# Performance work log

Hardware: AMD Instinct MI355X
Metric: run time of the kernel (lower is better)

Reference implementation:

```python
import jax, jax.numpy as jnp
import numpy as np

N_NODES, E, M_CELLS = 100000, 400000, 50000
D_IN, D_H, D_OUT = 384, 256, 256


def setup_inputs() -> dict:
    key = jax.random.key(0)
    ks = jax.random.split(key, 13)
    s = 0.02
    return {
        "chunk_features": jax.random.normal(ks[0], (N_NODES, D_IN), jnp.float32),
        "flat_nodes_t": jax.random.randint(ks[1], (E,), 0, N_NODES),
        "cell_asgn_t": jax.random.randint(ks[2], (E,), 0, M_CELLS),
        "M": M_CELLS,
        # phi: Linear(D_IN,D_H)+ReLU, Linear(D_H,D_H)+ReLU
        "W1": jax.random.normal(ks[3], (D_IN, D_H), jnp.float32) * s,
        "b1": jnp.zeros((D_H,), jnp.float32),
        "W2": jax.random.normal(ks[4], (D_H, D_H), jnp.float32) * s,
        "b2": jnp.zeros((D_H,), jnp.float32),
        # rho: Linear(D_H,D_H)+ReLU, Linear(D_H,D_H)+ReLU, Linear(D_H,D_OUT)
        "R1": jax.random.normal(ks[5], (D_H, D_H), jnp.float32) * s,
        "c1": jnp.zeros((D_H,), jnp.float32),
        "R2": jax.random.normal(ks[6], (D_H, D_H), jnp.float32) * s,
        "c2": jnp.zeros((D_H,), jnp.float32),
        "R3": jax.random.normal(ks[7], (D_H, D_OUT), jnp.float32) * s,
        "c3": jnp.zeros((D_OUT,), jnp.float32),
    }


def reference(chunk_features, flat_nodes_t, cell_asgn_t, M,
              W1, b1, W2, b2, R1, c1, R2, c2, R3, c3):
    # gather node features per cell-membership: [E, D_IN]
    x = chunk_features[flat_nodes_t]
    # phi MLP
    h = jax.nn.relu(x @ W1 + b1)
    h = jax.nn.relu(h @ W2 + b2)            # [E, D_H]
    # scatter-add per cell (torch scatter_add_ into zeros)
    cell_sums = jax.ops.segment_sum(h, cell_asgn_t, num_segments=M)  # [M, D_H]
    # rho MLP
    r = jax.nn.relu(cell_sums @ R1 + c1)
    r = jax.nn.relu(r @ R2 + c2)
    return r @ R3 + c3                      # [M, D_OUT]
```

## Files before the change

kernel.cpp:

```cpp
#include <hip/hip_runtime.h>

typedef unsigned short u16;
typedef __bf16 bf16x8 __attribute__((ext_vector_type(8)));
typedef float f32x4 __attribute__((ext_vector_type(4)));

__device__ __forceinline__ u16 f2bf(float f) {
  unsigned int u = __builtin_bit_cast(unsigned int, f);
  u += 0x7fffu + ((u >> 16) & 1u);
  return (u16)(u >> 16);
}
__device__ __forceinline__ float bf2f(u16 h) {
  unsigned int u = ((unsigned int)h) << 16;
  return __builtin_bit_cast(float, u);
}

__global__ __launch_bounds__(256) void k_prep(
    const float* __restrict__ W1, const float* __restrict__ W2,
    const float* __restrict__ R1, const float* __restrict__ R2, const float* __restrict__ R3,
    u16* __restrict__ W1s, u16* __restrict__ W2s,
    u16* __restrict__ R1s, u16* __restrict__ R2s, u16* __restrict__ R3s) {
  int t = blockIdx.x * 256 + threadIdx.x;
  const float* src; u16* dst; int lt;
  if (t < 12288) { src = W1; dst = W1s; lt = t; }
  else {
    int u = t - 12288;
    int m = u >> 13;
    lt = u & 8191;
    if (m == 0)      { src = W2; dst = W2s; }
    else if (m == 1) { src = R1; dst = R1s; }
    else if (m == 2) { src = R2; dst = R2s; }
    else if (m == 3) { src = R3; dst = R3s; }
    else return;
  }
  int lane = lt & 63;
  int nt = (lt >> 6) & 15;
  int ks = lt >> 10;
  int col = nt * 16 + (lane & 15);
  int kb = ks * 32 + (lane >> 4) * 8;
  union { u16 u[8]; uint4 v; } o;
#pragma unroll
  for (int j = 0; j < 8; ++j) o.u[j] = f2bf(src[(size_t)(kb + j) * 256 + col]);
  *(uint4*)(dst + (size_t)lt * 8) = o.v;
}

__global__ __launch_bounds__(256) void k_hist(const int* __restrict__ cells,
                                              int* __restrict__ counts, int E) {
  int e = blockIdx.x * 256 + threadIdx.x;
  if (e < E) atomicAdd(&counts[cells[e]], 1);
}

__global__ __launch_bounds__(256) void k_scan1(const int* __restrict__ counts,
                                               int* __restrict__ offs,
                                               int* __restrict__ bsum, int M) {
  __shared__ int ws[4];
  int tid = threadIdx.x, lane = tid & 63, wid = tid >> 6;
  int i = blockIdx.x * 256 + tid;
  int v = (i < M) ? counts[i] : 0;
  int x = v;
#pragma unroll
  for (int s = 1; s < 64; s <<= 1) { int y = __shfl_up(x, s); if (lane >= s) x += y; }
  if (lane == 63) ws[wid] = x;
  __syncthreads();
  int pre = 0;
#pragma unroll
  for (int w = 0; w < 4; ++w) if (w < wid) pre += ws[w];
  if (i < M) offs[i] = pre + x - v;
  if (tid == 255) bsum[blockIdx.x] = pre + x;
}

__global__ __launch_bounds__(256) void k_scan2(int* __restrict__ bsum, int nb) {
  __shared__ int ws[4];
  int tid = threadIdx.x, lane = tid & 63, wid = tid >> 6;
  int v = (tid < nb) ? bsum[tid] : 0;
  int x = v;
#pragma unroll
  for (int s = 1; s < 64; s <<= 1) { int y = __shfl_up(x, s); if (lane >= s) x += y; }
  if (lane == 63) ws[wid] = x;
  __syncthreads();
  int pre = 0;
#pragma unroll
  for (int w = 0; w < 4; ++w) if (w < wid) pre += ws[w];
  if (tid < nb) bsum[tid] = pre + x - v;
}

__global__ __launch_bounds__(256) void k_scan3(int* __restrict__ offs,
                                               const int* __restrict__ bsum,
                                               int* __restrict__ cursor, int M, int E) {
  int i = blockIdx.x * 256 + threadIdx.x;
  if (i < M) { int o = offs[i] + bsum[blockIdx.x]; offs[i] = o; cursor[i] = o; }
  if (i == M) offs[M] = E;
}

__global__ __launch_bounds__(256) void k_scatter(const int* __restrict__ cells,
                                                 const int* __restrict__ nodes,
                                                 int* __restrict__ cursor,
                                                 int* __restrict__ sorted, int E) {
  int e = blockIdx.x * 256 + threadIdx.x;
  if (e < E) {
    int c = cells[e];
    int p = atomicAdd(&cursor[c], 1);
    sorted[p] = nodes[e];
  }
}

__global__ __launch_bounds__(256) void k_phi(
    const float* __restrict__ X,
    const u16* __restrict__ W1s, const float* __restrict__ b1,
    const u16* __restrict__ W2s, const float* __restrict__ b2,
    u16* __restrict__ H, int N) {
  __shared__ __align__(16) u16 xbuf[32 * 384];
  __shared__ __align__(16) u16 hbuf[32 * 256];
  const int tid = threadIdx.x, lane = tid & 63, wid = tid >> 6;
  const int g = lane >> 4, r16 = lane & 15;
  const int swz = r16 << 3;
  const int T = (N + 31) >> 5;
  const int step = gridDim.x;

  const u16* w1p = W1s + (size_t)(wid * 4) * 512 + lane * 8;
  const u16* w2p = W2s + (size_t)(wid * 4) * 512 + lane * 8;

  float bias1[4], bias2[4];
#pragma unroll
  for (int n = 0; n < 4; ++n) {
    bias1[n] = b1[wid * 64 + n * 16 + r16];
    bias2[n] = b2[wid * 64 + n * 16 + r16];
  }

  f32x4 xr[12];

  auto issue = [&](int t) {
#pragma unroll
    for (int it = 0; it < 12; ++it) {
      int u = it * 256 + tid;
      int row = u / 96, c4 = u - row * 96;
      int crow = t * 32 + row; crow = crow < N ? crow : N - 1;
      xr[it] = *(const f32x4*)(X + (size_t)crow * 384 + c4 * 4);
    }
  };
  auto stagewrite = [&]() {
#pragma unroll
    for (int it = 0; it < 12; ++it) {
      int u = it * 256 + tid;
      int row = u / 96, c4 = u - row * 96;
      uint2 pk;
      pk.x = (unsigned int)f2bf(xr[it][0]) | ((unsigned int)f2bf(xr[it][1]) << 16);
      pk.y = (unsigned int)f2bf(xr[it][2]) | ((unsigned int)f2bf(xr[it][3]) << 16);
      *(uint2*)(xbuf + row * 384 + ((c4 * 4) ^ ((row & 15) << 3))) = pk;
    }
  };

  const int t0 = blockIdx.x;
  if (t0 >= T) return;

  issue(t0);
  stagewrite();
  __syncthreads();
  issue(t0 + step);

  for (int t = t0; t < T; t += step) {
    f32x4 acc[2][4];
#pragma unroll
    for (int m = 0; m < 2; ++m)
#pragma unroll
      for (int n = 0; n < 4; ++n) acc[m][n] = (f32x4){0.f, 0.f, 0.f, 0.f};
#pragma unroll 4
    for (int ks = 0; ks < 12; ++ks) {
      bf16x8 bfr[4];
#pragma unroll
      for (int n = 0; n < 4; ++n)
        bfr[n] = *(const bf16x8*)(w1p + (size_t)ks * 8192 + n * 512);
      const u16* bp = xbuf + ((ks * 32 + g * 8) ^ swz);
#pragma unroll
      for (int m = 0; m < 2; ++m) {
        bf16x8 af = *(const bf16x8*)(bp + (m * 16 + r16) * 384);
#pragma unroll
        for (int n = 0; n < 4; ++n)
          acc[m][n] = __builtin_amdgcn_mfma_f32_16x16x32_bf16(af, bfr[n], acc[m][n], 0, 0, 0);
      }
    }
    __syncthreads();

    stagewrite();

#pragma unroll
    for (int m = 0; m < 2; ++m)
#pragma unroll
      for (int n = 0; n < 4; ++n)
#pragma unroll
        for (int rr = 0; rr < 4; ++rr) {
          int row = m * 16 + g * 4 + rr;
          int col = wid * 64 + n * 16 + r16;
          float v = fmaxf(acc[m][n][rr] + bias1[n], 0.f);
          hbuf[row * 256 + (col ^ ((row & 15) << 3))] = f2bf(v);
        }
    __syncthreads();

    issue(t + 2 * step);

#pragma unroll
    for (int m = 0; m < 2; ++m)
#pragma unroll
      for (int n = 0; n < 4; ++n) acc[m][n] = (f32x4){0.f, 0.f, 0.f, 0.f};
#pragma unroll 4
    for (int ks = 0; ks < 8; ++ks) {
      bf16x8 bfr[4];
#pragma unroll
      for (int n = 0; n < 4; ++n)
        bfr[n] = *(const bf16x8*)(w2p + (size_t)ks * 8192 + n * 512);
      const u16* bp = hbuf + ((ks * 32 + g * 8) ^ swz);
#pragma unroll
      for (int m = 0; m < 2; ++m) {
        bf16x8 af = *(const bf16x8*)(bp + (m * 16 + r16) * 256);
#pragma unroll
        for (int n = 0; n < 4; ++n)
          acc[m][n] = __builtin_amdgcn_mfma_f32_16x16x32_bf16(af, bfr[n], acc[m][n], 0, 0, 0);
      }
    }
    __syncthreads();

#pragma unroll
    for (int m = 0; m < 2; ++m)
#pragma unroll
      for (int n = 0; n < 4; ++n)
#pragma unroll
        for (int rr = 0; rr < 4; ++rr) {
          int row = m * 16 + g * 4 + rr;
          int col = wid * 64 + n * 16 + r16;
          float v = fmaxf(acc[m][n][rr] + bias2[n], 0.f);
          hbuf[row * 256 + (col ^ ((row & 15) << 3))] = f2bf(v);
        }
    __syncthreads();

#pragma unroll
    for (int it = 0; it < 4; ++it) {
      int u = it * 256 + tid;
      int row = u >> 5, k8 = u & 31;
      uint4 d = *(const uint4*)(hbuf + row * 256 + ((k8 * 8) ^ ((row & 15) << 3)));
      int grow = t * 32 + row;
      if (grow < N) *(uint4*)(H + (size_t)grow * 256 + k8 * 8) = d;
    }
  }
}

__global__ __launch_bounds__(256) void k_cellsum(
    const u16* __restrict__ H, const int* __restrict__ sorted,
    const int* __restrict__ offs, u16* __restrict__ CS, int M) {
  const int lane = threadIdx.x & 63, wid = threadIdx.x >> 6;
  int c = blockIdx.x * 4 + wid;
  if (c >= M) return;
  int s = offs[c], e = offs[c + 1];
  float a0 = 0.f, a1 = 0.f, a2 = 0.f, a3 = 0.f;
  for (int base = s; base < e; base += 64) {
    int cnt = e - base; if (cnt > 64) cnt = 64;
    int idx = sorted[base + (lane < cnt ? lane : 0)];
    int j = 0;
    for (; j + 8 <= cnt; j += 8) {
      ushort4 h[8];
#pragma unroll
      for (int q = 0; q < 8; ++q) {
        int nd = __shfl(idx, j + q);
        h[q] = *(const ushort4*)(H + (size_t)nd * 256 + lane * 4);
      }
#pragma unroll
      for (int q = 0; q < 8; ++q) {
        a0 += bf2f(h[q].x); a1 += bf2f(h[q].y);
        a2 += bf2f(h[q].z); a3 += bf2f(h[q].w);
      }
    }
    if (j + 4 <= cnt) {
      ushort4 h[4];
#pragma unroll
      for (int q = 0; q < 4; ++q) {
        int nd = __shfl(idx, j + q);
        h[q] = *(const ushort4*)(H + (size_t)nd * 256 + lane * 4);
      }
#pragma unroll
      for (int q = 0; q < 4; ++q) {
        a0 += bf2f(h[q].x); a1 += bf2f(h[q].y);
        a2 += bf2f(h[q].z); a3 += bf2f(h[q].w);
      }
      j += 4;
    }
    for (; j < cnt; ++j) {
      int nd = __shfl(idx, j);
      ushort4 h = *(const ushort4*)(H + (size_t)nd * 256 + lane * 4);
      a0 += bf2f(h.x); a1 += bf2f(h.y); a2 += bf2f(h.z); a3 += bf2f(h.w);
    }
  }
  ushort4 o;
  o.x = f2bf(a0); o.y = f2bf(a1); o.z = f2bf(a2); o.w = f2bf(a3);
  *(ushort4*)(CS + (size_t)c * 256 + lane * 4) = o;
}

__global__ __launch_bounds__(256) void k_rho(
    const u16* __restrict__ CS,
    const u16* __restrict__ R1s, const float* __restrict__ c1,
    const u16* __restrict__ R2s, const float* __restrict__ c2,
    const u16* __restrict__ R3s, const float* __restrict__ c3,
    float* __restrict__ OUT, int M) {
  __shared__ __align__(16) u16 xbuf[32 * 256];
  __shared__ __align__(16) u16 hbuf[32 * 256];
  const int tid = threadIdx.x, lane = tid & 63, wid = tid >> 6;
  const int g = lane >> 4, r16 = lane & 15;
  const int swz = r16 << 3;
  const int T = (M + 31) >> 5;
  const int step = gridDim.x;

  const u16* w1p = R1s + (size_t)(wid * 4) * 512 + lane * 8;
  const u16* w2p = R2s + (size_t)(wid * 4) * 512 + lane * 8;
  const u16* w3p = R3s + (size_t)(wid * 4) * 512 + lane * 8;

  float bias1[4], bias2[4], bias3[4];
#pragma unroll
  for (int n = 0; n < 4; ++n) {
    bias1[n] = c1[wid * 64 + n * 16 + r16];
    bias2[n] = c2[wid * 64 + n * 16 + r16];
    bias3[n] = c3[wid * 64 + n * 16 + r16];
  }

  uint4 xr[4];
  auto issue = [&](int t) {
#pragma unroll
    for (int it = 0; it < 4; ++it) {
      int u = it * 256 + tid;
      int row = u >> 5, k8 = u & 31;
      int crow = t * 32 + row; crow = crow < M ? crow : M - 1;
      xr[it] = *(const uint4*)(CS + (size_t)crow * 256 + k8 * 8);
    }
  };
  auto stagewrite = [&]() {
#pragma unroll
    for (int it = 0; it < 4; ++it) {
      int u = it * 256 + tid;
      int row = u >> 5, k8 = u & 31;
      *(uint4*)(xbuf + row * 256 + ((k8 * 8) ^ ((row & 15) << 3))) = xr[it];
    }
  };

  const int t0 = blockIdx.x;
  if (t0 >= T) return;
  issue(t0);
  stagewrite();
  __syncthreads();
  issue(t0 + step);

  for (int t = t0; t < T; t += step) {
    f32x4 acc[2][4];

#pragma unroll
    for (int m = 0; m < 2; ++m)
#pragma unroll
      for (int n = 0; n < 4; ++n) acc[m][n] = (f32x4){0.f, 0.f, 0.f, 0.f};
#pragma unroll 4
    for (int ks = 0; ks < 8; ++ks) {
      bf16x8 bfr[4];
#pragma unroll
      for (int n = 0; n < 4; ++n)
        bfr[n] = *(const bf16x8*)(w1p + (size_t)ks * 8192 + n * 512);
      const u16* bp = xbuf + ((ks * 32 + g * 8) ^ swz);
#pragma unroll
      for (int m = 0; m < 2; ++m) {
        bf16x8 af = *(const bf16x8*)(bp + (m * 16 + r16) * 256);
#pragma unroll
        for (int n = 0; n < 4; ++n)
          acc[m][n] = __builtin_amdgcn_mfma_f32_16x16x32_bf16(af, bfr[n], acc[m][n], 0, 0, 0);
      }
    }
    __syncthreads();

    stagewrite();

#pragma unroll
    for (int m = 0; m < 2; ++m)
#pragma unroll
      for (int n = 0; n < 4; ++n)
#pragma unroll
        for (int rr = 0; rr < 4; ++rr) {
          int row = m * 16 + g * 4 + rr;
          int col = wid * 64 + n * 16 + r16;
          float v = fmaxf(acc[m][n][rr] + bias1[n], 0.f);
          hbuf[row * 256 + (col ^ ((row & 15) << 3))] = f2bf(v);
        }
    __syncthreads();

    issue(t + 2 * step);

#pragma unroll
    for (int m = 0; m < 2; ++m)
#pragma unroll
      for (int n = 0; n < 4; ++n) acc[m][n] = (f32x4){0.f, 0.f, 0.f, 0.f};
#pragma unroll 4
    for (int ks = 0; ks < 8; ++ks) {
      bf16x8 bfr[4];
#pragma unroll
      for (int n = 0; n < 4; ++n)
        bfr[n] = *(const bf16x8*)(w2p + (size_t)ks * 8192 + n * 512);
      const u16* bp = hbuf + ((ks * 32 + g * 8) ^ swz);
#pragma unroll
      for (int m = 0; m < 2; ++m) {
        bf16x8 af = *(const bf16x8*)(bp + (m * 16 + r16) * 256);
#pragma unroll
        for (int n = 0; n < 4; ++n)
          acc[m][n] = __builtin_amdgcn_mfma_f32_16x16x32_bf16(af, bfr[n], acc[m][n], 0, 0, 0);
      }
    }
    __syncthreads();

#pragma unroll
    for (int m = 0; m < 2; ++m)
#pragma unroll
      for (int n = 0; n < 4; ++n)
#pragma unroll
        for (int rr = 0; rr < 4; ++rr) {
          int row = m * 16 + g * 4 + rr;
          int col = wid * 64 + n * 16 + r16;
          float v = fmaxf(acc[m][n][rr] + bias2[n], 0.f);
          hbuf[row * 256 + (col ^ ((row & 15) << 3))] = f2bf(v);
        }
    __syncthreads();

#pragma unroll
    for (int m = 0; m < 2; ++m)
#pragma unroll
      for (int n = 0; n < 4; ++n) acc[m][n] = (f32x4){0.f, 0.f, 0.f, 0.f};
#pragma unroll 4
    for (int ks = 0; ks < 8; ++ks) {
      bf16x8 bfr[4];
#pragma unroll
      for (int n = 0; n < 4; ++n)
        bfr[n] = *(const bf16x8*)(w3p + (size_t)ks * 8192 + n * 512);
      const u16* bp = hbuf + ((ks * 32 + g * 8) ^ swz);
#pragma unroll
      for (int m = 0; m < 2; ++m) {
        bf16x8 af = *(const bf16x8*)(bp + (m * 16 + r16) * 256);
#pragma unroll
        for (int n = 0; n < 4; ++n)
          acc[m][n] = __builtin_amdgcn_mfma_f32_16x16x32_bf16(af, bfr[n], acc[m][n], 0, 0, 0);
      }
    }
#pragma unroll
    for (int n = 0; n < 4; ++n) {
#pragma unroll
      for (int m = 0; m < 2; ++m)
#pragma unroll
        for (int rr = 0; rr < 4; ++rr) {
          int grow = t * 32 + m * 16 + g * 4 + rr;
          if (grow < M)
            OUT[(size_t)grow * 256 + wid * 64 + n * 16 + r16] = acc[m][n][rr] + bias3[n];
        }
    }
  }
}

extern "C" void kernel_launch(void* const* d_in, const int* in_sizes, int n_in,
                              void* d_out, int out_size, void* d_ws, size_t ws_size,
                              hipStream_t stream) {
  const float* X    = (const float*)d_in[0];
  const int* nodes  = (const int*)d_in[1];
  const int* cells  = (const int*)d_in[2];
  const float* W1   = (const float*)d_in[4];
  const float* b1   = (const float*)d_in[5];
  const float* W2   = (const float*)d_in[6];
  const float* b2   = (const float*)d_in[7];
  const float* R1   = (const float*)d_in[8];
  const float* c1   = (const float*)d_in[9];
  const float* R2   = (const float*)d_in[10];
  const float* c2   = (const float*)d_in[11];
  const float* R3   = (const float*)d_in[12];
  const float* c3   = (const float*)d_in[13];
  float* OUT = (float*)d_out;

  const int N = in_sizes[0] / 384;
  const int E = in_sizes[1];
  const int M = out_size / 256;

  char* ws = (char*)d_ws;
  size_t off = 0;
  auto alloc = [&](size_t b) { size_t o = off; off += (b + 255) & ~(size_t)255; return o; };
  u16* W1s    = (u16*)(ws + alloc((size_t)12 * 16 * 64 * 8 * 2));
  u16* W2s    = (u16*)(ws + alloc((size_t)8 * 16 * 64 * 8 * 2));
  u16* R1s    = (u16*)(ws + alloc((size_t)8 * 16 * 64 * 8 * 2));
  u16* R2s    = (u16*)(ws + alloc((size_t)8 * 16 * 64 * 8 * 2));
  u16* R3s    = (u16*)(ws + alloc((size_t)8 * 16 * 64 * 8 * 2));
  u16* H      = (u16*)(ws + alloc((size_t)N * 256 * 2));
  u16* CS     = (u16*)(ws + alloc((size_t)M * 256 * 2));
  int* counts = (int*)(ws + alloc((size_t)M * 4));
  int* offs   = (int*)(ws + alloc((size_t)(M + 1) * 4));
  int* cursor = (int*)(ws + alloc((size_t)M * 4));
  int* sorted = (int*)(ws + alloc((size_t)E * 4));
  int* bsum   = (int*)(ws + alloc((size_t)256 * 4));

  const int NB = (M + 255) / 256;

  hipMemsetAsync(counts, 0, (size_t)M * 4, stream);
  k_prep<<<176, 256, 0, stream>>>(W1, W2, R1, R2, R3, W1s, W2s, R1s, R2s, R3s);
  k_hist<<<(E + 255) / 256, 256, 0, stream>>>(cells, counts, E);
  k_scan1<<<NB, 256, 0, stream>>>(counts, offs, bsum, M);
  k_scan2<<<1, 256, 0, stream>>>(bsum, NB);
  k_scan3<<<(M + 256) / 256, 256, 0, stream>>>(offs, bsum, cursor, M, E);
  k_scatter<<<(E + 255) / 256, 256, 0, stream>>>(cells, nodes, cursor, sorted, E);
  k_phi<<<1024, 256, 0, stream>>>(X, W1s, b1, W2s, b2, H, N);
  k_cellsum<<<(M + 3) / 4, 256, 0, stream>>>(H, sorted, offs, CS, M);
  k_rho<<<512, 256, 0, stream>>>(CS, R1s, c1, R2s, c2, R3s, c3, OUT, M);
}
```

Before: 219.0 us.

## Split phi MLP into two persistent kernels with weights resident in LDS

The fused phi kernel is split into two persistent kernels, one per layer, each running 256 blocks at one block per CU. Each block copies its layer's bf16 weights into shared memory (the last third of W1 is held in registers), so weights no longer have to be re-read from global or L2 on every tile. The price is an extra round trip of the N×256 bf16 intermediate through global memory, an extra launch, and lower occupancy that leaves less latency hiding.

```diff
diff --git a/kernel.cpp b/kernel.cpp
--- a/kernel.cpp
+++ b/kernel.cpp
@@ -103,31 +103,36 @@
   }
 }
 
-__global__ __launch_bounds__(256) void k_phi(
+__global__ __launch_bounds__(256, 1) void k_phi_l1(
     const float* __restrict__ X,
     const u16* __restrict__ W1s, const float* __restrict__ b1,
-    const u16* __restrict__ W2s, const float* __restrict__ b2,
-    u16* __restrict__ H, int N) {
+    u16* __restrict__ P, int N) {
+  __shared__ __align__(16) u16 wlds[65536];
   __shared__ __align__(16) u16 xbuf[32 * 384];
-  __shared__ __align__(16) u16 hbuf[32 * 256];
   const int tid = threadIdx.x, lane = tid & 63, wid = tid >> 6;
   const int g = lane >> 4, r16 = lane & 15;
   const int swz = r16 << 3;
   const int T = (N + 31) >> 5;
   const int step = gridDim.x;
 
-  const u16* w1p = W1s + (size_t)(wid * 4) * 512 + lane * 8;
-  const u16* w2p = W2s + (size_t)(wid * 4) * 512 + lane * 8;
-
-  float bias1[4], bias2[4];
-#pragma unroll
-  for (int n = 0; n < 4; ++n) {
-    bias1[n] = b1[wid * 64 + n * 16 + r16];
-    bias2[n] = b2[wid * 64 + n * 16 + r16];
-  }
+  {
+    const uint4* wsrc = (const uint4*)W1s;
+    uint4* wdst = (uint4*)wlds;
+#pragma unroll
+    for (int i = 0; i < 32; ++i) wdst[i * 256 + tid] = wsrc[i * 256 + tid];
+  }
+  bf16x8 ksr[4][4];
+#pragma unroll
+  for (int k2 = 0; k2 < 4; ++k2)
+#pragma unroll
+    for (int n = 0; n < 4; ++n)
+      ksr[k2][n] = *(const bf16x8*)(W1s + ((size_t)((8 + k2) * 16 + wid * 4 + n) * 64 + lane) * 8);
+
+  float bias1[4];
+#pragma unroll
+  for (int n = 0; n < 4; ++n) bias1[n] = b1[wid * 64 + n * 16 + r16];
 
   f32x4 xr[12];
-
   auto issue = [&](int t) {
 #pragma unroll
     for (int it = 0; it < 12; ++it) {
@@ -151,24 +156,25 @@
 
   const int t0 = blockIdx.x;
   if (t0 >= T) return;
-
   issue(t0);
-  stagewrite();
-  __syncthreads();
-  issue(t0 + step);
 
   for (int t = t0; t < T; t += step) {
+    stagewrite();
+    __syncthreads();
+    issue(t + step);
+
     f32x4 acc[2][4];
 #pragma unroll
     for (int m = 0; m < 2; ++m)
 #pragma unroll
       for (int n = 0; n < 4; ++n) acc[m][n] = (f32x4){0.f, 0.f, 0.f, 0.f};
-#pragma unroll 4
-    for (int ks = 0; ks < 12; ++ks) {
+
+#pragma unroll 2
+    for (int ks = 0; ks < 8; ++ks) {
       bf16x8 bfr[4];
 #pragma unroll
       for (int n = 0; n < 4; ++n)
-        bfr[n] = *(const bf16x8*)(w1p + (size_t)ks * 8192 + n * 512);
+        bfr[n] = *(const bf16x8*)(wlds + ((ks * 16 + wid * 4 + n) * 64 + lane) * 8);
       const u16* bp = xbuf + ((ks * 32 + g * 8) ^ swz);
 #pragma unroll
       for (int m = 0; m < 2; ++m) {
@@ -178,9 +184,18 @@
           acc[m][n] = __builtin_amdgcn_mfma_f32_16x16x32_bf16(af, bfr[n], acc[m][n], 0, 0, 0);
       }
     }
-    __syncthreads();
-
-    stagewrite();
+#pragma unroll
+    for (int k2 = 0; k2 < 4; ++k2) {
+      const u16* bp = xbuf + (((8 + k2) * 32 + g * 8) ^ swz);
+#pragma unroll
+      for (int m = 0; m < 2; ++m) {
+        bf16x8 af = *(const bf16x8*)(bp + (m * 16 + r16) * 384);
+#pragma unroll
+        for (int n = 0; n < 4; ++n)
+          acc[m][n] = __builtin_amdgcn_mfma_f32_16x16x32_bf16(af, ksr[k2][n], acc[m][n], 0, 0, 0);
+      }
+    }
+    __syncthreads();
 
 #pragma unroll
     for (int m = 0; m < 2; ++m)
@@ -191,23 +206,83 @@
           int row = m * 16 + g * 4 + rr;
           int col = wid * 64 + n * 16 + r16;
           float v = fmaxf(acc[m][n][rr] + bias1[n], 0.f);
-          hbuf[row * 256 + (col ^ ((row & 15) << 3))] = f2bf(v);
+          xbuf[row * 256 + (col ^ ((row & 15) << 3))] = f2bf(v);
         }
     __syncthreads();
 
-    issue(t + 2 * step);
-
+#pragma unroll
+    for (int it = 0; it < 4; ++it) {
+      int u = it * 256 + tid;
+      int row = u >> 5, k8 = u & 31;
+      uint4 d = *(const uint4*)(xbuf + row * 256 + ((k8 * 8) ^ ((row & 15) << 3)));
+      int grow = t * 32 + row;
+      if (grow < N) *(uint4*)(P + (size_t)grow * 256 + k8 * 8) = d;
+    }
+    __syncthreads();
+  }
+}
+
+__global__ __launch_bounds__(256, 1) void k_phi_l2(
+    const u16* __restrict__ W2s, const float* __restrict__ b2,
+    u16* __restrict__ P, int N) {
+  __shared__ __align__(16) u16 wlds[65536];
+  __shared__ __align__(16) u16 xbuf[32 * 256];
+  const int tid = threadIdx.x, lane = tid & 63, wid = tid >> 6;
+  const int g = lane >> 4, r16 = lane & 15;
+  const int swz = r16 << 3;
+  const int T = (N + 31) >> 5;
+  const int step = gridDim.x;
+
+  {
+    const uint4* wsrc = (const uint4*)W2s;
+    uint4* wdst = (uint4*)wlds;
+#pragma unroll
+    for (int i = 0; i < 32; ++i) wdst[i * 256 + tid] = wsrc[i * 256 + tid];
+  }
+  float bias2[4];
+#pragma unroll
+  for (int n = 0; n < 4; ++n) bias2[n] = b2[wid * 64 + n * 16 + r16];
+
+  uint4 xr[4];
+  auto issue = [&](int t) {
+#pragma unroll
+    for (int it = 0; it < 4; ++it) {
+      int u = it * 256 + tid;
+      int row = u >> 5, k8 = u & 31;
+      int crow = t * 32 + row; crow = crow < N ? crow : N - 1;
+      xr[it] = *(const uint4*)(P + (size_t)crow * 256 + k8 * 8);
+    }
+  };
+  auto stagewrite = [&]() {
+#pragma unroll
+    for (int it = 0; it < 4; ++it) {
+      int u = it * 256 + tid;
+      int row = u >> 5, k8 = u & 31;
+      *(uint4*)(xbuf + row * 256 + ((k8 * 8) ^ ((row & 15) << 3))) = xr[it];
+    }
+  };
+
+  const int t0 = blockIdx.x;
+  if (t0 >= T) return;
+  issue(t0);
+
+  for (int t = t0; t < T; t += step) {
+    stagewrite();
+    __syncthreads();
+    issue(t + step);
+
+    f32x4 acc[2][4];
 #pragma unroll
     for (int m = 0; m < 2; ++m)
 #pragma unroll
       for (int n = 0; n < 4; ++n) acc[m][n] = (f32x4){0.f, 0.f, 0.f, 0.f};
-#pragma unroll 4
+#pragma unroll 2
     for (int ks = 0; ks < 8; ++ks) {
       bf16x8 bfr[4];
 #pragma unroll
       for (int n = 0; n < 4; ++n)
-        bfr[n] = *(const bf16x8*)(w2p + (size_t)ks * 8192 + n * 512);
-      const u16* bp = hbuf + ((ks * 32 + g * 8) ^ swz);
+        bfr[n] = *(const bf16x8*)(wlds + ((ks * 16 + wid * 4 + n) * 64 + lane) * 8);
+      const u16* bp = xbuf + ((ks * 32 + g * 8) ^ swz);
 #pragma unroll
       for (int m = 0; m < 2; ++m) {
         bf16x8 af = *(const bf16x8*)(bp + (m * 16 + r16) * 256);
@@ -227,7 +302,7 @@
           int row = m * 16 + g * 4 + rr;
           int col = wid * 64 + n * 16 + r16;
           float v = fmaxf(acc[m][n][rr] + bias2[n], 0.f);
-          hbuf[row * 256 + (col ^ ((row & 15) << 3))] = f2bf(v);
+          xbuf[row * 256 + (col ^ ((row & 15) << 3))] = f2bf(v);
         }
     __syncthreads();
 
@@ -235,10 +310,11 @@
     for (int it = 0; it < 4; ++it) {
       int u = it * 256 + tid;
       int row = u >> 5, k8 = u & 31;
-      uint4 d = *(const uint4*)(hbuf + row * 256 + ((k8 * 8) ^ ((row & 15) << 3)));
+      uint4 d = *(const uint4*)(xbuf + row * 256 + ((k8 * 8) ^ ((row & 15) << 3)));
       int grow = t * 32 + row;
-      if (grow < N) *(uint4*)(H + (size_t)grow * 256 + k8 * 8) = d;
-    }
+      if (grow < N) *(uint4*)(P + (size_t)grow * 256 + k8 * 8) = d;
+    }
+    __syncthreads();
   }
 }
 
@@ -482,7 +558,7 @@
   u16* R1s    = (u16*)(ws + alloc((size_t)8 * 16 * 64 * 8 * 2));
   u16* R2s    = (u16*)(ws + alloc((size_t)8 * 16 * 64 * 8 * 2));
   u16* R3s    = (u16*)(ws + alloc((size_t)8 * 16 * 64 * 8 * 2));
-  u16* H      = (u16*)(ws + alloc((size_t)N * 256 * 2));
+  u16* P      = (u16*)(ws + alloc((size_t)N * 256 * 2));
   u16* CS     = (u16*)(ws + alloc((size_t)M * 256 * 2));
   int* counts = (int*)(ws + alloc((size_t)M * 4));
   int* offs   = (int*)(ws + alloc((size_t)(M + 1) * 4));
@@ -499,7 +575,8 @@
   k_scan2<<<1, 256, 0, stream>>>(bsum, NB);
   k_scan3<<<(M + 256) / 256, 256, 0, stream>>>(offs, bsum, cursor, M, E);
   k_scatter<<<(E + 255) / 256, 256, 0, stream>>>(cells, nodes, cursor, sorted, E);
-  k_phi<<<1024, 256, 0, stream>>>(X, W1s, b1, W2s, b2, H, N);
-  k_cellsum<<<(M + 3) / 4, 256, 0, stream>>>(H, sorted, offs, CS, M);
+  k_phi_l1<<<256, 256, 0, stream>>>(X, W1s, b1, P, N);
+  k_phi_l2<<<256, 256, 0, stream>>>(W2s, b2, P, N);
+  k_cellsum<<<(M + 3) / 4, 256, 0, stream>>>(P, sorted, offs, CS, M);
   k_rho<<<512, 256, 0, stream>>>(CS, R1s, c1, R2s, c2, R3s, c3, OUT, M);
 }
```

Result: slower. 247.9 us (+13.2%).

## Split fused phi and rho MLP kernels into per-layer non-persistent kernels

Applied to the files above, without the earlier changes.

Replaces the persistent, software-prefetched k_phi and k_rho kernels with one kernel per linear layer (k_l1, k_b2b, k_lout), each processing a single 32-row tile per block. Intermediate activations are now round-tripped through global bf16 buffers (h1buf, RB) instead of staying in shared memory. The aim is likely higher occupancy, since each kernel uses less LDS and a simpler body. The cost is extra global memory traffic, more launches, loss of load/compute overlap, and narrow scattered bf16 stores. One launch also passes RB as both source and destination of a __restrict__ kernel.

```diff
diff --git a/kernel.cpp b/kernel.cpp
--- a/kernel.cpp
+++ b/kernel.cpp
@@ -103,41 +103,27 @@
   }
 }
 
-__global__ __launch_bounds__(256) void k_phi(
+__global__ __launch_bounds__(256) void k_l1(
     const float* __restrict__ X,
     const u16* __restrict__ W1s, const float* __restrict__ b1,
-    const u16* __restrict__ W2s, const float* __restrict__ b2,
-    u16* __restrict__ H, int N) {
+    u16* __restrict__ h1, int N) {
   __shared__ __align__(16) u16 xbuf[32 * 384];
-  __shared__ __align__(16) u16 hbuf[32 * 256];
   const int tid = threadIdx.x, lane = tid & 63, wid = tid >> 6;
   const int g = lane >> 4, r16 = lane & 15;
   const int swz = r16 << 3;
-  const int T = (N + 31) >> 5;
-  const int step = gridDim.x;
-
-  const u16* w1p = W1s + (size_t)(wid * 4) * 512 + lane * 8;
-  const u16* w2p = W2s + (size_t)(wid * 4) * 512 + lane * 8;
-
-  float bias1[4], bias2[4];
-#pragma unroll
-  for (int n = 0; n < 4; ++n) {
-    bias1[n] = b1[wid * 64 + n * 16 + r16];
-    bias2[n] = b2[wid * 64 + n * 16 + r16];
-  }
-
-  f32x4 xr[12];
-
-  auto issue = [&](int t) {
+  const int rbase = blockIdx.x * 32;
+
+  const u16* wp = W1s + (size_t)(wid * 4) * 512 + lane * 8;
+
+  {
+    f32x4 xr[12];
 #pragma unroll
     for (int it = 0; it < 12; ++it) {
       int u = it * 256 + tid;
       int row = u / 96, c4 = u - row * 96;
-      int crow = t * 32 + row; crow = crow < N ? crow : N - 1;
+      int crow = rbase + row; crow = crow < N ? crow : N - 1;
       xr[it] = *(const f32x4*)(X + (size_t)crow * 384 + c4 * 4);
     }
-  };
-  auto stagewrite = [&]() {
 #pragma unroll
     for (int it = 0; it < 12; ++it) {
       int u = it * 256 + tid;
@@ -147,99 +133,184 @@
       pk.y = (unsigned int)f2bf(xr[it][2]) | ((unsigned int)f2bf(xr[it][3]) << 16);
       *(uint2*)(xbuf + row * 384 + ((c4 * 4) ^ ((row & 15) << 3))) = pk;
     }
-  };
-
-  const int t0 = blockIdx.x;
-  if (t0 >= T) return;
-
-  issue(t0);
-  stagewrite();
+  }
   __syncthreads();
-  issue(t0 + step);
-
-  for (int t = t0; t < T; t += step) {
-    f32x4 acc[2][4];
-#pragma unroll
-    for (int m = 0; m < 2; ++m)
-#pragma unroll
-      for (int n = 0; n < 4; ++n) acc[m][n] = (f32x4){0.f, 0.f, 0.f, 0.f};
+
+  f32x4 acc[2][4];
+#pragma unroll
+  for (int m = 0; m < 2; ++m)
+#pragma unroll
+    for (int n = 0; n < 4; ++n) acc[m][n] = (f32x4){0.f, 0.f, 0.f, 0.f};
+
 #pragma unroll 4
-    for (int ks = 0; ks < 12; ++ks) {
-      bf16x8 bfr[4];
+  for (int ks = 0; ks < 12; ++ks) {
+    bf16x8 bfr[4];
+#pragma unroll
+    for (int n = 0; n < 4; ++n)
+      bfr[n] = *(const bf16x8*)(wp + (size_t)ks * 8192 + n * 512);
+    const u16* bp = xbuf + ((ks * 32 + g * 8) ^ swz);
+#pragma unroll
+    for (int m = 0; m < 2; ++m) {
+      bf16x8 af = *(const bf16x8*)(bp + (m * 16 + r16) * 384);
 #pragma unroll
       for (int n = 0; n < 4; ++n)
-        bfr[n] = *(const bf16x8*)(w1p + (size_t)ks * 8192 + n * 512);
-      const u16* bp = xbuf + ((ks * 32 + g * 8) ^ swz);
-#pragma unroll
-      for (int m = 0; m < 2; ++m) {
-        bf16x8 af = *(const bf16x8*)(bp + (m * 16 + r16) * 384);
+        acc[m][n] = __builtin_amdgcn_mfma_f32_16x16x32_bf16(af, bfr[n], acc[m][n], 0, 0, 0);
+    }
+  }
+
+  float bias[4];
+#pragma unroll
+  for (int n = 0; n < 4; ++n) bias[n] = b1[wid * 64 + n * 16 + r16];
+#pragma unroll
+  for (int m = 0; m < 2; ++m)
+#pragma unroll
+    for (int rr = 0; rr < 4; ++rr) {
+      int grow = rbase + m * 16 + g * 4 + rr;
+      if (grow < N) {
+        u16* op = h1 + (size_t)grow * 256 + wid * 64 + r16;
 #pragma unroll
         for (int n = 0; n < 4; ++n)
-          acc[m][n] = __builtin_amdgcn_mfma_f32_16x16x32_bf16(af, bfr[n], acc[m][n], 0, 0, 0);
-      }
-    }
-    __syncthreads();
-
-    stagewrite();
-
-#pragma unroll
-    for (int m = 0; m < 2; ++m)
+          op[n * 16] = f2bf(fmaxf(acc[m][n][rr] + bias[n], 0.f));
+      }
+    }
+}
+
+__global__ __launch_bounds__(256) void k_b2b(
+    const u16* __restrict__ src,
+    const u16* __restrict__ Ws, const float* __restrict__ b,
+    u16* __restrict__ dst, int R) {
+  __shared__ __align__(16) u16 xbuf[32 * 256];
+  const int tid = threadIdx.x, lane = tid & 63, wid = tid >> 6;
+  const int g = lane >> 4, r16 = lane & 15;
+  const int swz = r16 << 3;
+  const int rbase = blockIdx.x * 32;
+
+  const u16* wp = Ws + (size_t)(wid * 4) * 512 + lane * 8;
+
+  {
+    uint4 xr[4];
+#pragma unroll
+    for (int it = 0; it < 4; ++it) {
+      int u = it * 256 + tid;
+      int row = u >> 5, k8 = u & 31;
+      int crow = rbase + row; crow = crow < R ? crow : R - 1;
+      xr[it] = *(const uint4*)(src + (size_t)crow * 256 + k8 * 8);
+    }
+#pragma unroll
+    for (int it = 0; it < 4; ++it) {
+      int u = it * 256 + tid;
+      int row = u >> 5, k8 = u & 31;
+      *(uint4*)(xbuf + row * 256 + ((k8 * 8) ^ ((row & 15) << 3))) = xr[it];
+    }
+  }
+  __syncthreads();
+
+  f32x4 acc[2][4];
+#pragma unroll
+  for (int m = 0; m < 2; ++m)
+#pragma unroll
+    for (int n = 0; n < 4; ++n) acc[m][n] = (f32x4){0.f, 0.f, 0.f, 0.f};
+
+#pragma unroll 4
+  for (int ks = 0; ks < 8; ++ks) {
+    bf16x8 bfr[4];
+#pragma unroll
+    for (int n = 0; n < 4; ++n)
+      bfr[n] = *(const bf16x8*)(wp + (size_t)ks * 8192 + n * 512);
+    const u16* bp = xbuf + ((ks * 32 + g * 8) ^ swz);
+#pragma unroll
+    for (int m = 0; m < 2; ++m) {
+      bf16x8 af = *(const bf16x8*)(bp + (m * 16 + r16) * 256);
 #pragma unroll
       for (int n = 0; n < 4; ++n)
-#pragma unroll
-        for (int rr = 0; rr < 4; ++rr) {
-          int row = m * 16 + g * 4 + rr;
-          int col = wid * 64 + n * 16 + r16;
-          float v = fmaxf(acc[m][n][rr] + bias1[n], 0.f);
-          hbuf[row * 256 + (col ^ ((row & 15) << 3))] = f2bf(v);
-        }
-    __syncthreads();
-
-    issue(t + 2 * step);
-
-#pragma unroll
-    for (int m = 0; m < 2; ++m)
-#pragma unroll
-      for (int n = 0; n < 4; ++n) acc[m][n] = (f32x4){0.f, 0.f, 0.f, 0.f};
+        acc[m][n] = __builtin_amdgcn_mfma_f32_16x16x32_bf16(af, bfr[n], acc[m][n], 0, 0, 0);
+    }
+  }
+
+  float bias[4];
+#pragma unroll
+  for (int n = 0; n < 4; ++n) bias[n] = b[wid * 64 + n * 16 + r16];
+#pragma unroll
+  for (int m = 0; m < 2; ++m)
+#pragma unroll
+    for (int rr = 0; rr < 4; ++rr) {
+      int grow = rbase + m * 16 + g * 4 + rr;
+      if (grow < R) {
+        u16* op = dst + (size_t)grow * 256 + wid * 64 + r16;
+#pragma unroll
+        for (int n = 0; n < 4; ++n)
+          op[n * 16] = f2bf(fmaxf(acc[m][n][rr] + bias[n], 0.f));
+      }
+    }
+}
+
+__global__ __launch_bounds__(256) void k_lout(
+    const u16* __restrict__ src,
+    const u16* __restrict__ Ws, const float* __restrict__ b,
+    float* __restrict__ OUT, int R) {
+  __shared__ __align__(16) u16 xbuf[32 * 256];
+  const int tid = threadIdx.x, lane = tid & 63, wid = tid >> 6;
+  const int g = lane >> 4, r16 = lane & 15;
+  const int swz = r16 << 3;
+  const int rbase = blockIdx.x * 32;
+
+  const u16* wp = Ws + (size_t)(wid * 4) * 512 + lane * 8;
+
+  {
+    uint4 xr[4];
+#pragma unroll
+    for (int it = 0; it < 4; ++it) {
+      int u = it * 256 + tid;
+      int row = u >> 5, k8 = u & 31;
+      int crow = rbase + row; crow = crow < R ? crow : R - 1;
+      xr[it] = *(const uint4*)(src + (size_t)crow * 256 + k8 * 8);
+    }
+#pragma unroll
+    for (int it = 0; it < 4; ++it) {
+      int u = it * 256 + tid;
+      int row = u >> 5, k8 = u & 31;
+      *(uint4*)(xbuf + row * 256 + ((k8 * 8) ^ ((row & 15) << 3))) = xr[it];
+    }
+  }
+  __syncthreads();
+
+  f32x4 acc[2][4];
+#pragma unroll
+  for (int m = 0; m < 2; ++m)
+#pragma unroll
+    for (int n = 0; n < 4; ++n) acc[m][n] = (f32x4){0.f, 0.f, 0.f, 0.f};
+
 #pragma unroll 4
-    for (int ks = 0; ks < 8; ++ks) {
-      bf16x8 bfr[4];
+  for (int ks = 0; ks < 8; ++ks) {
+    bf16x8 bfr[4];
+#pragma unroll
+    for (int n = 0; n < 4; ++n)
+      bfr[n] = *(const bf16x8*)(wp + (size_t)ks * 8192 + n * 512);
+    const u16* bp = xbuf + ((ks * 32 + g * 8) ^ swz);
+#pragma unroll
+    for (int m = 0; m < 2; ++m) {
+      bf16x8 af = *(const bf16x8*)(bp + (m * 16 + r16) * 256);
 #pragma unroll
       for (int n = 0; n < 4; ++n)
-        bfr[n] = *(const bf16x8*)(w2p + (size_t)ks * 8192 + n * 512);
-      const u16* bp = hbuf + ((ks * 32 + g * 8) ^ swz);
-#pragma unroll
-      for (int m = 0; m < 2; ++m) {
-        bf16x8 af = *(const bf16x8*)(bp + (m * 16 + r16) * 256);
+        acc[m][n] = __builtin_amdgcn_mfma_f32_16x16x32_bf16(af, bfr[n], acc[m][n], 0, 0, 0);
+    }
+  }
+
+  float bias[4];
+#pragma unroll
+  for (int n = 0; n < 4; ++n) bias[n] = b[wid * 64 + n * 16 + r16];
+#pragma unroll
+  for (int m = 0; m < 2; ++m)
+#pragma unroll
+    for (int rr = 0; rr < 4; ++rr) {
+      int grow = rbase + m * 16 + g * 4 + rr;
+      if (grow < R) {
+        float* op = OUT + (size_t)grow * 256 + wid * 64 + r16;
 #pragma unroll
         for (int n = 0; n < 4; ++n)
-          acc[m][n] = __builtin_amdgcn_mfma_f32_16x16x32_bf16(af, bfr[n], acc[m][n], 0, 0, 0);
-      }
-    }
-    __syncthreads();
-
-#pragma unroll
-    for (int m = 0; m < 2; ++m)
-#pragma unroll
-      for (int n = 0; n < 4; ++n)
-#pragma unroll
-        for (int rr = 0; rr < 4; ++rr) {
-          int row = m * 16 + g * 4 + rr;
-          int col = wid * 64 + n * 16 + r16;
-          float v = fmaxf(acc[m][n][rr] + bias2[n], 0.f);
-          hbuf[row * 256 + (col ^ ((row & 15) << 3))] = f2bf(v);
-        }
-    __syncthreads();
-
-#pragma unroll
-    for (int it = 0; it < 4; ++it) {
-      int u = it * 256 + tid;
-      int row = u >> 5, k8 = u & 31;
-      uint4 d = *(const uint4*)(hbuf + row * 256 + ((k8 * 8) ^ ((row & 15) << 3)));
-      int grow = t * 32 + row;
-      if (grow < N) *(uint4*)(H + (size_t)grow * 256 + k8 * 8) = d;
-    }
-  }
+          op[n * 16] = acc[m][n][rr] + bias[n];
+      }
+    }
 }
 
 __global__ __launch_bounds__(256) void k_cellsum(
@@ -290,166 +361,6 @@
   ushort4 o;
   o.x = f2bf(a0); o.y = f2bf(a1); o.z = f2bf(a2); o.w = f2bf(a3);
   *(ushort4*)(CS + (size_t)c * 256 + lane * 4) = o;
-}
-
-__global__ __launch_bounds__(256) void k_rho(
-    const u16* __restrict__ CS,
-    const u16* __restrict__ R1s, const float* __restrict__ c1,
-    const u16* __restrict__ R2s, const float* __restrict__ c2,
-    const u16* __restrict__ R3s, const float* __restrict__ c3,
-    float* __restrict__ OUT, int M) {
-  __shared__ __align__(16) u16 xbuf[32 * 256];
-  __shared__ __align__(16) u16 hbuf[32 * 256];
-  const int tid = threadIdx.x, lane = tid & 63, wid = tid >> 6;
-  const int g = lane >> 4, r16 = lane & 15;
-  const int swz = r16 << 3;
-  const int T = (M + 31) >> 5;
-  const int step = gridDim.x;
-
-  const u16* w1p = R1s + (size_t)(wid * 4) * 512 + lane * 8;
-  const u16* w2p = R2s + (size_t)(wid * 4) * 512 + lane * 8;
-  const u16* w3p = R3s + (size_t)(wid * 4) * 512 + lane * 8;
-
-  float bias1[4], bias2[4], bias3[4];
-#pragma unroll
-  for (int n = 0; n < 4; ++n) {
-    bias1[n] = c1[wid * 64 + n * 16 + r16];
-    bias2[n] = c2[wid * 64 + n * 16 + r16];
-    bias3[n] = c3[wid * 64 + n * 16 + r16];
-  }
-
-  uint4 xr[4];
-  auto issue = [&](int t) {
-#pragma unroll
-    for (int it = 0; it < 4; ++it) {
-      int u = it * 256 + tid;
-      int row = u >> 5, k8 = u & 31;
-      int crow = t * 32 + row; crow = crow < M ? crow : M - 1;
-      xr[it] = *(const uint4*)(CS + (size_t)crow * 256 + k8 * 8);
-    }
-  };
-  auto stagewrite = [&]() {
-#pragma unroll
-    for (int it = 0; it < 4; ++it) {
-      int u = it * 256 + tid;
-      int row = u >> 5, k8 = u & 31;
-      *(uint4*)(xbuf + row * 256 + ((k8 * 8) ^ ((row & 15) << 3))) = xr[it];
-    }
-  };
-
-  const int t0 = blockIdx.x;
-  if (t0 >= T) return;
-  issue(t0);
-  stagewrite();
-  __syncthreads();
-  issue(t0 + step);
-
-  for (int t = t0; t < T; t += step) {
-    f32x4 acc[2][4];
-
-#pragma unroll
-    for (int m = 0; m < 2; ++m)
-#pragma unroll
-      for (int n = 0; n < 4; ++n) acc[m][n] = (f32x4){0.f, 0.f, 0.f, 0.f};
-#pragma unroll 4
-    for (int ks = 0; ks < 8; ++ks) {
-      bf16x8 bfr[4];
-#pragma unroll
-      for (int n = 0; n < 4; ++n)
-        bfr[n] = *(const bf16x8*)(w1p + (size_t)ks * 8192 + n * 512);
-      const u16* bp = xbuf + ((ks * 32 + g * 8) ^ swz);
-#pragma unroll
-      for (int m = 0; m < 2; ++m) {
-        bf16x8 af = *(const bf16x8*)(bp + (m * 16 + r16) * 256);
-#pragma unroll
-        for (int n = 0; n < 4; ++n)
-          acc[m][n] = __builtin_amdgcn_mfma_f32_16x16x32_bf16(af, bfr[n], acc[m][n], 0, 0, 0);
-      }
-    }
-    __syncthreads();
-
-    stagewrite();
-
-#pragma unroll
-    for (int m = 0; m < 2; ++m)
-#pragma unroll
-      for (int n = 0; n < 4; ++n)
-#pragma unroll
-        for (int rr = 0; rr < 4; ++rr) {
-          int row = m * 16 + g * 4 + rr;
-          int col = wid * 64 + n * 16 + r16;
-          float v = fmaxf(acc[m][n][rr] + bias1[n], 0.f);
-          hbuf[row * 256 + (col ^ ((row & 15) << 3))] = f2bf(v);
-        }
-    __syncthreads();
-
-    issue(t + 2 * step);
-
-#pragma unroll
-    for (int m = 0; m < 2; ++m)
-#pragma unroll
-      for (int n = 0; n < 4; ++n) acc[m][n] = (f32x4){0.f, 0.f, 0.f, 0.f};
-#pragma unroll 4
-    for (int ks = 0; ks < 8; ++ks) {
-      bf16x8 bfr[4];
-#pragma unroll
-      for (int n = 0; n < 4; ++n)
-        bfr[n] = *(const bf16x8*)(w2p + (size_t)ks * 8192 + n * 512);
-      const u16* bp = hbuf + ((ks * 32 + g * 8) ^ swz);
-#pragma unroll
-      for (int m = 0; m < 2; ++m) {
-        bf16x8 af = *(const bf16x8*)(bp + (m * 16 + r16) * 256);
-#pragma unroll
-        for (int n = 0; n < 4; ++n)
-          acc[m][n] = __builtin_amdgcn_mfma_f32_16x16x32_bf16(af, bfr[n], acc[m][n], 0, 0, 0);
-      }
-    }
-    __syncthreads();
-
-#pragma unroll
-    for (int m = 0; m < 2; ++m)
-#pragma unroll
-      for (int n = 0; n < 4; ++n)
-#pragma unroll
-        for (int rr = 0; rr < 4; ++rr) {
-          int row = m * 16 + g * 4 + rr;
-          int col = wid * 64 + n * 16 + r16;
-          float v = fmaxf(acc[m][n][rr] + bias2[n], 0.f);
-          hbuf[row * 256 + (col ^ ((row & 15) << 3))] = f2bf(v);
-        }
-    __syncthreads();
-
-#pragma unroll
-    for (int m = 0; m < 2; ++m)
-#pragma unroll
-      for (int n = 0; n < 4; ++n) acc[m][n] = (f32x4){0.f, 0.f, 0.f, 0.f};
-#pragma unroll 4
-    for (int ks = 0; ks < 8; ++ks) {
-      bf16x8 bfr[4];
-#pragma unroll
-      for (int n = 0; n < 4; ++n)
-        bfr[n] = *(const bf16x8*)(w3p + (size_t)ks * 8192 + n * 512);
-      const u16* bp = hbuf + ((ks * 32 + g * 8) ^ swz);
-#pragma unroll
-      for (int m = 0; m < 2; ++m) {
-        bf16x8 af = *(const bf16x8*)(bp + (m * 16 + r16) * 256);
-#pragma unroll
-        for (int n = 0; n < 4; ++n)
-          acc[m][n] = __builtin_amdgcn_mfma_f32_16x16x32_bf16(af, bfr[n], acc[m][n], 0, 0, 0);
-      }
-    }
-#pragma unroll
-    for (int n = 0; n < 4; ++n) {
-#pragma unroll
-      for (int m = 0; m < 2; ++m)
-#pragma unroll
-        for (int rr = 0; rr < 4; ++rr) {
-          int grow = t * 32 + m * 16 + g * 4 + rr;
-          if (grow < M)
-            OUT[(size_t)grow * 256 + wid * 64 + n * 16 + r16] = acc[m][n][rr] + bias3[n];
-        }
-    }
-  }
 }
 
 extern "C" void kernel_launch(void* const* d_in, const int* in_sizes, int n_in,
@@ -482,8 +393,10 @@
   u16* R1s    = (u16*)(ws + alloc((size_t)8 * 16 * 64 * 8 * 2));
   u16* R2s    = (u16*)(ws + alloc((size_t)8 * 16 * 64 * 8 * 2));
   u16* R3s    = (u16*)(ws + alloc((size_t)8 * 16 * 64 * 8 * 2));
+  u16* h1buf  = (u16*)(ws + alloc((size_t)N * 256 * 2));
   u16* H      = (u16*)(ws + alloc((size_t)N * 256 * 2));
   u16* CS     = (u16*)(ws + alloc((size_t)M * 256 * 2));
+  u16* RB     = (u16*)(ws + alloc((size_t)M * 256 * 2));
   int* counts = (int*)(ws + alloc((size_t)M * 4));
   int* offs   = (int*)(ws + alloc((size_t)(M + 1) * 4));
   int* cursor = (int*)(ws + alloc((size_t)M * 4));
@@ -491,6 +404,8 @@
   int* bsum   = (int*)(ws + alloc((size_t)256 * 4));
 
   const int NB = (M + 255) / 256;
+  const int TN = (N + 31) / 32;
+  const int TM = (M + 31) / 32;
 
   hipMemsetAsync(counts, 0, (size_t)M * 4, stream);
   k_prep<<<176, 256, 0, stream>>>(W1, W2, R1, R2, R3, W1s, W2s, R1s, R2s, R3s);
@@ -499,7 +414,10 @@
   k_scan2<<<1, 256, 0, stream>>>(bsum, NB);
   k_scan3<<<(M + 256) / 256, 256, 0, stream>>>(offs, bsum, cursor, M, E);
   k_scatter<<<(E + 255) / 256, 256, 0, stream>>>(cells, nodes, cursor, sorted, E);
-  k_phi<<<1024, 256, 0, stream>>>(X, W1s, b1, W2s, b2, H, N);
+  k_l1<<<TN, 256, 0, stream>>>(X, W1s, b1, h1buf, N);
+  k_b2b<<<TN, 256, 0, stream>>>(h1buf, W2s, b2, H, N);
   k_cellsum<<<(M + 3) / 4, 256, 0, stream>>>(H, sorted, offs, CS, M);
-  k_rho<<<512, 256, 0, stream>>>(CS, R1s, c1, R2s, c2, R3s, c3, OUT, M);
-}
+  k_b2b<<<TM, 256, 0, stream>>>(CS, R1s, c1, RB, M);
+  k_b2b<<<TM, 256, 0, stream>>>(RB, R2s, c2, RB, M);
+  k_lout<<<TM, 256, 0, stream>>>(RB, R3s, c3, OUT, M);
+}
```

Result: slower. 237.8 us (+8.6%).
